# Optimization experiments

Measured on AMD Instinct MI355X. Metric: run time of the kernel, lower is better.

The kernel has to match this reference:

```python
import jax, jax.numpy as jnp
import numpy as np
from jax import lax

FS = 100.0
N_FILT = 12
N_CHANNELS = 27
FILT_DIM = 5
MIN_FREQ = 1.0


def setup_inputs() -> dict:
    key = jax.random.key(0)
    k1, k2, k3 = jax.random.split(key, 3)
    x = jax.random.normal(k1, (8, N_CHANNELS, 65536), dtype=jnp.float32)
    filt_low = jax.random.uniform(k2, (N_CHANNELS, N_FILT), dtype=jnp.float32)
    filt_band = jax.random.uniform(k3, (N_CHANNELS, N_FILT), dtype=jnp.float32)
    return {"x": x, "filt_low": filt_low, "filt_band": filt_band}


def _low_pass(freq, t_right):
    # freq: [C, F] normalized cutoff; t_right: [(FILT_DIM-1)//2] (already / fs)
    # Sinc.forward: sin(2*pi*band*t)/(2*pi*band*t) with band = freq*fs
    arg = (2.0 * jnp.pi * FS) * freq[..., None] * t_right      # [C, F, T2]
    y_right = jnp.sin(arg) / arg                                # [C, F, T2]
    ones = jnp.ones(freq.shape + (1,), dtype=freq.dtype)
    y = jnp.concatenate([y_right[..., ::-1], ones, y_right], axis=-1)  # [C, F, FILT_DIM]
    return 2.0 * freq[..., None] * y


def _build_filters(filt_low, filt_band):
    beg = jnp.abs(filt_low) + MIN_FREQ / FS                     # [C, F]
    end = beg + jnp.abs(filt_band)                              # [C, F]
    half = (FILT_DIM - 1) // 2
    t_right = jnp.linspace(1.0, (FILT_DIM - 1) / 2.0, half) / FS
    band_pass = _low_pass(end, t_right) - _low_pass(beg, t_right)  # [C, F, FILT_DIM]
    band_pass = band_pass / jnp.max(band_pass, axis=-1, keepdims=True)
    # Blackman-ish window, faithful to torch.linspace(0, Filt_dim, Filt_dim)
    n = jnp.linspace(0.0, float(FILT_DIM), FILT_DIM)
    window = (0.42 - 0.5 * jnp.cos(2.0 * jnp.pi * n / FILT_DIM)
              + 0.08 * jnp.cos(4.0 * jnp.pi * n / FILT_DIM))
    filters = band_pass * window                                # [C, F, FILT_DIM]
    # row order k = j*N_filt + i matches grouped-conv output ordering
    return filters.reshape(N_CHANNELS * N_FILT, 1, FILT_DIM)


def reference(x, filt_low, filt_band):
    filters = _build_filters(filt_low, filt_band)               # [C*F, 1, K]
    out = lax.conv_general_dilated(
        x, filters,
        window_strides=(1,), padding='VALID',
        dimension_numbers=('NCH', 'OIH', 'NCH'),
        feature_group_count=N_CHANNELS)
    return out  # [B, C*F, T-K+1]
```

## Files before the change

kernel.cpp:

```cpp
#include <hip/hip_runtime.h>
#include <math.h>

#define NF 12
#define NC 27
#define KD 5
#define T_IN 65536
#define T_OUT 65532
#define TILE 1024

__global__ __launch_bounds__(256) void sinc_conv_kernel(
    const float* __restrict__ x,
    const float* __restrict__ flow,
    const float* __restrict__ fband,
    float* __restrict__ out)
{
    __shared__ float sf[NF][KD];

    const int tid = threadIdx.x;
    const int c  = blockIdx.y;
    const int b  = blockIdx.z;

    if (tid < NF) {
        const float PI = 3.14159265358979323846f;
        float lo = fabsf(flow[c * NF + tid]) + 0.01f;
        float hi = lo + fabsf(fband[c * NF + tid]);

        float bp[KD];
        bp[2] = 2.0f * hi - 2.0f * lo;
        #pragma unroll
        for (int j = 1; j <= 2; ++j) {
            float ah = 2.0f * PI * hi * (float)j;
            float al = 2.0f * PI * lo * (float)j;
            float v = 2.0f * hi * (sinf(ah) / ah) - 2.0f * lo * (sinf(al) / al);
            bp[2 + j] = v;
            bp[2 - j] = v;
        }
        float mx = bp[0];
        #pragma unroll
        for (int k = 1; k < KD; ++k) mx = fmaxf(mx, bp[k]);

        #pragma unroll
        for (int k = 0; k < KD; ++k) {
            float n = 1.25f * (float)k;
            float win = 0.42f - 0.5f * cosf(2.0f * PI * n / 5.0f)
                              + 0.08f * cosf(4.0f * PI * n / 5.0f);
            sf[tid][k] = (bp[k] / mx) * win;
        }
    }
    __syncthreads();

    const int t0 = blockIdx.x * TILE + tid * 4;
    if (t0 >= T_OUT) return;

    const float* xrow = x + (size_t)(b * NC + c) * T_IN;
    const float4* x4 = (const float4*)xrow;
    float4 A = x4[t0 >> 2];
    float4 B = x4[(t0 >> 2) + 1];
    float xv0 = A.x, xv1 = A.y, xv2 = A.z, xv3 = A.w;
    float xv4 = B.x, xv5 = B.y, xv6 = B.z, xv7 = B.w;

    float* obase = out + (size_t)(b * NC + c) * NF * T_OUT;

    #pragma unroll
    for (int f = 0; f < NF; ++f) {
        float w0 = sf[f][0], w1 = sf[f][1], w2 = sf[f][2], w3 = sf[f][3], w4 = sf[f][4];
        float4 o;
        o.x = xv0 * w0 + xv1 * w1 + xv2 * w2 + xv3 * w3 + xv4 * w4;
        o.y = xv1 * w0 + xv2 * w1 + xv3 * w2 + xv4 * w3 + xv5 * w4;
        o.z = xv2 * w0 + xv3 * w1 + xv4 * w2 + xv5 * w3 + xv6 * w4;
        o.w = xv3 * w0 + xv4 * w1 + xv5 * w2 + xv6 * w3 + xv7 * w4;
        float4* orow = (float4*)(obase + (size_t)f * T_OUT);
        orow[t0 >> 2] = o;
    }
}

extern "C" void kernel_launch(void* const* d_in, const int* in_sizes, int n_in,
                              void* d_out, int out_size, void* d_ws, size_t ws_size,
                              hipStream_t stream) {
    const float* x     = (const float*)d_in[0];
    const float* flow  = (const float*)d_in[1];
    const float* fband = (const float*)d_in[2];
    float* out = (float*)d_out;

    dim3 grid((T_IN + TILE - 1) / TILE, NC, 8);
    dim3 block(256);
    sinc_conv_kernel<<<grid, block, 0, stream>>>(x, flow, fband, out);
}
```

Measured before the change: 725.8 us.

## Drop zero-window taps, process four chunks per thread, precompute filters

The window is zero at both ends (k=0 and k=4), so the convolution keeps only the three middle taps. That cuts the multiply-adds per output from five to three. Each thread now loads four 1024-sample chunks and writes 12×4 float4 outputs, with 4096 samples per block and a quarter as many blocks. When workspace is available, a separate tiny kernel builds the filter table once into it, instead of every block recomputing taps with sin and cos. The costs are an extra kernel launch and higher register pressure. Also, the end taps are not bit-exactly zero in float, so dropping them is a tiny numerical approximation.

```diff
diff --git a/kernel.cpp b/kernel.cpp
--- a/kernel.cpp
+++ b/kernel.cpp
@@ -6,83 +6,163 @@
 #define KD 5
 #define T_IN 65536
 #define T_OUT 65532
-#define TILE 1024
+#define CHUNKS 4
+#define TILE 4096
 
-__global__ __launch_bounds__(256) void sinc_conv_kernel(
+__device__ __forceinline__ float4 make_taps(float lo_in, float band_in)
+{
+    const float PI = 3.14159265358979323846f;
+    float lo = fabsf(lo_in) + 0.01f;
+    float hi = lo + fabsf(band_in);
+
+    float bp[KD];
+    bp[2] = 2.0f * hi - 2.0f * lo;
+    #pragma unroll
+    for (int j = 1; j <= 2; ++j) {
+        float ah = 2.0f * PI * hi * (float)j;
+        float al = 2.0f * PI * lo * (float)j;
+        float v = 2.0f * hi * (sinf(ah) / ah) - 2.0f * lo * (sinf(al) / al);
+        bp[2 + j] = v;
+        bp[2 - j] = v;
+    }
+    float mx = bp[0];
+    #pragma unroll
+    for (int k = 1; k < KD; ++k) mx = fmaxf(mx, bp[k]);
+
+    float w[3];
+    #pragma unroll
+    for (int k = 1; k <= 3; ++k) {
+        float n = 1.25f * (float)k;
+        float win = 0.42f - 0.5f * cosf(2.0f * PI * n / 5.0f)
+                          + 0.08f * cosf(4.0f * PI * n / 5.0f);
+        w[k - 1] = (bp[k] / mx) * win;
+    }
+    return make_float4(w[0], w[1], w[2], 0.0f);
+}
+
+__global__ void build_filters(const float* __restrict__ flow,
+                              const float* __restrict__ fband,
+                              float4* __restrict__ wtab)
+{
+    int i = blockIdx.x * blockDim.x + threadIdx.x;
+    if (i < NC * NF) wtab[i] = make_taps(flow[i], fband[i]);
+}
+
+__global__ __launch_bounds__(256) void sinc_conv_ws(
+    const float* __restrict__ x,
+    const float4* __restrict__ wtab,
+    float* __restrict__ out)
+{
+    const int tid  = threadIdx.x;
+    const int c    = blockIdx.y;
+    const int b    = blockIdx.z;
+    const int tile = blockIdx.x * TILE;
+
+    const float4* __restrict__ x4 =
+        (const float4*)(x + (size_t)(b * NC + c) * T_IN);
+
+    float xa[CHUNKS][8];
+    int   ia[CHUNKS];
+    bool  ok[CHUNKS];
+    #pragma unroll
+    for (int ch = 0; ch < CHUNKS; ++ch) {
+        int t = tile + ch * 1024 + (tid << 2);
+        int i = t >> 2;
+        ok[ch] = (t < T_OUT);
+        ia[ch] = i;
+        float4 A = x4[i];
+        float4 B = x4[ok[ch] ? i + 1 : i];
+        xa[ch][0] = A.x; xa[ch][1] = A.y; xa[ch][2] = A.z; xa[ch][3] = A.w;
+        xa[ch][4] = B.x; xa[ch][5] = B.y; xa[ch][6] = B.z; xa[ch][7] = B.w;
+    }
+
+    float* obase = out + (size_t)(b * NC + c) * NF * T_OUT;
+    const float4* __restrict__ wt = wtab + c * NF;
+
+    #pragma unroll
+    for (int f = 0; f < NF; ++f) {
+        const float4 w = wt[f];
+        float4* orow = (float4*)(obase + (size_t)f * T_OUT);
+        #pragma unroll
+        for (int ch = 0; ch < CHUNKS; ++ch) {
+            float4 o;
+            o.x = xa[ch][1] * w.x + xa[ch][2] * w.y + xa[ch][3] * w.z;
+            o.y = xa[ch][2] * w.x + xa[ch][3] * w.y + xa[ch][4] * w.z;
+            o.z = xa[ch][3] * w.x + xa[ch][4] * w.y + xa[ch][5] * w.z;
+            o.w = xa[ch][4] * w.x + xa[ch][5] * w.y + xa[ch][6] * w.z;
+            if (ok[ch]) orow[ia[ch]] = o;
+        }
+    }
+}
+
+__global__ __launch_bounds__(256) void sinc_conv_fb(
     const float* __restrict__ x,
     const float* __restrict__ flow,
     const float* __restrict__ fband,
     float* __restrict__ out)
 {
-    __shared__ float sf[NF][KD];
+    __shared__ float4 sw[NF];
+    const int tid  = threadIdx.x;
+    const int c    = blockIdx.y;
+    const int b    = blockIdx.z;
+    const int tile = blockIdx.x * TILE;
 
-    const int tid = threadIdx.x;
-    const int c  = blockIdx.y;
-    const int b  = blockIdx.z;
-
-    if (tid < NF) {
-        const float PI = 3.14159265358979323846f;
-        float lo = fabsf(flow[c * NF + tid]) + 0.01f;
-        float hi = lo + fabsf(fband[c * NF + tid]);
-
-        float bp[KD];
-        bp[2] = 2.0f * hi - 2.0f * lo;
-        #pragma unroll
-        for (int j = 1; j <= 2; ++j) {
-            float ah = 2.0f * PI * hi * (float)j;
-            float al = 2.0f * PI * lo * (float)j;
-            float v = 2.0f * hi * (sinf(ah) / ah) - 2.0f * lo * (sinf(al) / al);
-            bp[2 + j] = v;
-            bp[2 - j] = v;
-        }
-        float mx = bp[0];
-        #pragma unroll
-        for (int k = 1; k < KD; ++k) mx = fmaxf(mx, bp[k]);
-
-        #pragma unroll
-        for (int k = 0; k < KD; ++k) {
-            float n = 1.25f * (float)k;
-            float win = 0.42f - 0.5f * cosf(2.0f * PI * n / 5.0f)
-                              + 0.08f * cosf(4.0f * PI * n / 5.0f);
-            sf[tid][k] = (bp[k] / mx) * win;
-        }
-    }
+    if (tid < NF) sw[tid] = make_taps(flow[c * NF + tid], fband[c * NF + tid]);
     __syncthreads();
 
-    const int t0 = blockIdx.x * TILE + tid * 4;
-    if (t0 >= T_OUT) return;
+    const float4* __restrict__ x4 =
+        (const float4*)(x + (size_t)(b * NC + c) * T_IN);
 
-    const float* xrow = x + (size_t)(b * NC + c) * T_IN;
-    const float4* x4 = (const float4*)xrow;
-    float4 A = x4[t0 >> 2];
-    float4 B = x4[(t0 >> 2) + 1];
-    float xv0 = A.x, xv1 = A.y, xv2 = A.z, xv3 = A.w;
-    float xv4 = B.x, xv5 = B.y, xv6 = B.z, xv7 = B.w;
+    float xa[CHUNKS][8];
+    int   ia[CHUNKS];
+    bool  ok[CHUNKS];
+    #pragma unroll
+    for (int ch = 0; ch < CHUNKS; ++ch) {
+        int t = tile + ch * 1024 + (tid << 2);
+        int i = t >> 2;
+        ok[ch] = (t < T_OUT);
+        ia[ch] = i;
+        float4 A = x4[i];
+        float4 B = x4[ok[ch] ? i + 1 : i];
+        xa[ch][0] = A.x; xa[ch][1] = A.y; xa[ch][2] = A.z; xa[ch][3] = A.w;
+        xa[ch][4] = B.x; xa[ch][5] = B.y; xa[ch][6] = B.z; xa[ch][7] = B.w;
+    }
 
     float* obase = out + (size_t)(b * NC + c) * NF * T_OUT;
 
     #pragma unroll
     for (int f = 0; f < NF; ++f) {
-        float w0 = sf[f][0], w1 = sf[f][1], w2 = sf[f][2], w3 = sf[f][3], w4 = sf[f][4];
-        float4 o;
-        o.x = xv0 * w0 + xv1 * w1 + xv2 * w2 + xv3 * w3 + xv4 * w4;
-        o.y = xv1 * w0 + xv2 * w1 + xv3 * w2 + xv4 * w3 + xv5 * w4;
-        o.z = xv2 * w0 + xv3 * w1 + xv4 * w2 + xv5 * w3 + xv6 * w4;
-        o.w = xv3 * w0 + xv4 * w1 + xv5 * w2 + xv6 * w3 + xv7 * w4;
+        const float4 w = sw[f];
         float4* orow = (float4*)(obase + (size_t)f * T_OUT);
-        orow[t0 >> 2] = o;
+        #pragma unroll
+        for (int ch = 0; ch < CHUNKS; ++ch) {
+            float4 o;
+            o.x = xa[ch][1] * w.x + xa[ch][2] * w.y + xa[ch][3] * w.z;
+            o.y = xa[ch][2] * w.x + xa[ch][3] * w.y + xa[ch][4] * w.z;
+            o.z = xa[ch][3] * w.x + xa[ch][4] * w.y + xa[ch][5] * w.z;
+            o.w = xa[ch][4] * w.x + xa[ch][5] * w.y + xa[ch][6] * w.z;
+            if (ok[ch]) orow[ia[ch]] = o;
+        }
     }
 }
 
 extern "C" void kernel_launch(void* const* d_in, const int* in_sizes, int n_in,
                               void* d_out, int out_size, void* d_ws, size_t ws_size,
-                              hipStream_t stream) {
+                              hipStream_t stream)
+{
     const float* x     = (const float*)d_in[0];
     const float* flow  = (const float*)d_in[1];
     const float* fband = (const float*)d_in[2];
     float* out = (float*)d_out;
+    (void)in_sizes; (void)n_in; (void)out_size;
 
-    dim3 grid((T_IN + TILE - 1) / TILE, NC, 8);
+    dim3 grid(T_IN / TILE, NC, 8);
     dim3 block(256);
-    sinc_conv_kernel<<<grid, block, 0, stream>>>(x, flow, fband, out);
+
+    if (ws_size >= (size_t)(NC * NF) * sizeof(float4)) {
+        build_filters<<<1, 384, 0, stream>>>(flow, fband, (float4*)d_ws);
+        sinc_conv_ws<<<grid, block, 0, stream>>>(x, (const float4*)d_ws, out);
+    } else {
+        sinc_conv_fb<<<grid, block, 0, stream>>>(x, flow, fband, out);
+    }
 }
```

Measured after the change: 714.2 us. No clear change (-1.6%).
